# Optimization experiments

Measured on AMD Instinct MI355X. Metric: run time of the kernel, lower is better.

## Reference

```python
import jax, jax.numpy as jnp
import numpy as np
from jax.lax import associative_scan

D_H = 1024

def _binary_operator(e_i, e_j):
    a_i, kv_i = e_i
    a_j, kv_j = e_j
    return (a_j * a_i, a_j * kv_i + kv_j)

def setup_inputs() -> dict:
    key = jax.random.key(0)
    k1, k2 = jax.random.split(key)
    x = jax.random.normal(k1, (4, 4096, 3 * D_H), dtype=jnp.float32)
    carry = jax.random.normal(k2, (4, D_H), dtype=jnp.float32)
    return {"x": x, "carry": carry}

def reference(x, carry):
    d_h = D_H
    inp = jnp.tanh(x[:, :, :d_h])                      # (B, S, d_h)
    gates = jax.nn.sigmoid(x[:, :, d_h:])              # (B, S, 2*d_h)
    input_gate, output_gate = jnp.split(gates, 2, axis=-1)
    forget_gate = 1.0 - input_gate                     # tied gates
    scan_ins = inp * input_gate                        # (B, S, d_h)
    # inject carry at t=0: h_0 = f_0*carry + i_0*in_0
    scan_ins = scan_ins.at[:, 0, :].set(scan_ins[:, 0, :] + carry * forget_gate[:, 0, :])
    _, h = associative_scan(_binary_operator, (forget_gate, scan_ins), axis=1)
    y = jnp.tanh(h) * output_gate                      # (B, S, d_h)
    h_last = h[:, -1, :]
    return (h_last, y)
```

## Files before the change

### kernel.cpp

```cpp
#include <hip/hip_runtime.h>


#define B_SZ 4
#define T_LEN 4096
#define DH 1024
#define ROW4 (3 * DH / 4)
#define CHUNKS 128
#define CLEN (T_LEN / CHUNKS)

__device__ __forceinline__ float fsig(float v) {
    return __builtin_amdgcn_rcpf(1.0f + __expf(-v));
}
__device__ __forceinline__ float ftanh(float v) {
    return 1.0f - 2.0f * __builtin_amdgcn_rcpf(__expf(2.0f * v) + 1.0f);
}

__global__ __launch_bounds__(256) void glru_pass1(const float* __restrict__ x,
                                                  float4* __restrict__ Aag,
                                                  float4* __restrict__ Bag) {
    const int c = blockIdx.x;
    const int b = blockIdx.y;
    const int d4 = threadIdx.x;
    const float4* base = (const float4*)x + (size_t)(b * T_LEN + c * CLEN) * ROW4;

    float4 A = make_float4(1.f, 1.f, 1.f, 1.f);
    float4 Bv = make_float4(0.f, 0.f, 0.f, 0.f);
    for (int t = 0; t < CLEN; ++t) {
        const float4 vi = base[(size_t)t * ROW4 + d4];
        const float4 vg = base[(size_t)t * ROW4 + 256 + d4];
        {
            float ig = fsig(vg.x); float a = 1.f - ig;
            A.x *= a; Bv.x = a * Bv.x + ftanh(vi.x) * ig;
        }
        {
            float ig = fsig(vg.y); float a = 1.f - ig;
            A.y *= a; Bv.y = a * Bv.y + ftanh(vi.y) * ig;
        }
        {
            float ig = fsig(vg.z); float a = 1.f - ig;
            A.z *= a; Bv.z = a * Bv.z + ftanh(vi.z) * ig;
        }
        {
            float ig = fsig(vg.w); float a = 1.f - ig;
            A.w *= a; Bv.w = a * Bv.w + ftanh(vi.w) * ig;
        }
    }
    const int o = (b * CHUNKS + c) * 256 + d4;
    Aag[o] = A;
    Bag[o] = Bv;
}

__global__ __launch_bounds__(256) void glru_pass2(const float* __restrict__ Aag,
                                                  const float* __restrict__ Bag,
                                                  const float* __restrict__ carry,
                                                  float* __restrict__ hinit,
                                                  float* __restrict__ hlast) {
    const int idx = blockIdx.x * 256 + threadIdx.x;
    const int b = idx >> 10;
    const int d = idx & 1023;
    float h = carry[idx];
    #pragma unroll 8
    for (int c = 0; c < CHUNKS; ++c) {
        const int o = (b * CHUNKS + c) * 1024 + d;
        hinit[o] = h;
        h = Aag[o] * h + Bag[o];
    }
    hlast[idx] = h;
}

__global__ __launch_bounds__(256) void glru_pass3(const float* __restrict__ x,
                                                  const float4* __restrict__ hinit,
                                                  float4* __restrict__ y) {
    const int c = blockIdx.x;
    const int b = blockIdx.y;
    const int d4 = threadIdx.x;
    const float4* base = (const float4*)x + (size_t)(b * T_LEN + c * CLEN) * ROW4;
    float4* yb = y + (size_t)(b * T_LEN + c * CLEN) * 256;

    float4 h = hinit[(b * CHUNKS + c) * 256 + d4];
    for (int t = 0; t < CLEN; ++t) {
        const float4 vi = base[(size_t)t * ROW4 + d4];
        const float4 vg = base[(size_t)t * ROW4 + 256 + d4];
        const float4 vo = base[(size_t)t * ROW4 + 512 + d4];
        float4 out;
        {
            float ig = fsig(vg.x); float a = 1.f - ig;
            h.x = a * h.x + ftanh(vi.x) * ig;
            out.x = ftanh(h.x) * fsig(vo.x);
        }
        {
            float ig = fsig(vg.y); float a = 1.f - ig;
            h.y = a * h.y + ftanh(vi.y) * ig;
            out.y = ftanh(h.y) * fsig(vo.y);
        }
        {
            float ig = fsig(vg.z); float a = 1.f - ig;
            h.z = a * h.z + ftanh(vi.z) * ig;
            out.z = ftanh(h.z) * fsig(vo.z);
        }
        {
            float ig = fsig(vg.w); float a = 1.f - ig;
            h.w = a * h.w + ftanh(vi.w) * ig;
            out.w = ftanh(h.w) * fsig(vo.w);
        }
        yb[(size_t)t * 256 + d4] = out;
    }
}

extern "C" void kernel_launch(void* const* d_in, const int* in_sizes, int n_in,
                              void* d_out, int out_size, void* d_ws, size_t ws_size,
                              hipStream_t stream) {
    const float* x = (const float*)d_in[0];
    const float* carry = (const float*)d_in[1];

    float* hlast = (float*)d_out;
    float4* y = (float4*)((float*)d_out + B_SZ * DH);

    float* Aag = (float*)d_ws;
    float* Bag = Aag + (size_t)B_SZ * CHUNKS * DH;
    float* hinit = Bag + (size_t)B_SZ * CHUNKS * DH;

    glru_pass1<<<dim3(CHUNKS, B_SZ), 256, 0, stream>>>(x, (float4*)Aag, (float4*)Bag);
    glru_pass2<<<16, 256, 0, stream>>>(Aag, Bag, carry, hinit, hlast);
    glru_pass3<<<dim3(CHUNKS, B_SZ), 256, 0, stream>>>(x, (const float4*)hinit, y);
}
```

Before: 317.2 us.

## Double the chunk count, software-prefetch next timestep, and use nontemporal y stores

Raises CHUNKS from 128 to 256, which halves the sequential length per block and doubles the grid size for passes 1 and 3 so more waves can hide latency. The inner loops of pass1 and pass3 now load the next timestep's inputs before computing the current one, so load latency overlaps the transcendental math. The y output in pass3 is written with nontemporal stores to keep the streamed output from polluting cache. The cost is a longer serial scan in pass2 (256 chunks), more workspace traffic, and more registers held for the prefetched values.

```diff
diff --git a/kernel.cpp b/kernel.cpp
--- a/kernel.cpp
+++ b/kernel.cpp
@@ -5,8 +5,10 @@
 #define T_LEN 4096
 #define DH 1024
 #define ROW4 (3 * DH / 4)
-#define CHUNKS 128
+#define CHUNKS 256
 #define CLEN (T_LEN / CHUNKS)
+
+typedef float vf4 __attribute__((ext_vector_type(4)));
 
 __device__ __forceinline__ float fsig(float v) {
     return __builtin_amdgcn_rcpf(1.0f + __expf(-v));
@@ -25,9 +27,14 @@
 
     float4 A = make_float4(1.f, 1.f, 1.f, 1.f);
     float4 Bv = make_float4(0.f, 0.f, 0.f, 0.f);
+
+    float4 vi = base[d4];
+    float4 vg = base[256 + d4];
     for (int t = 0; t < CLEN; ++t) {
-        const float4 vi = base[(size_t)t * ROW4 + d4];
-        const float4 vg = base[(size_t)t * ROW4 + 256 + d4];
+        float4 vi_n, vg_n;
+        const int tn = (t + 1 < CLEN) ? (t + 1) : t;
+        vi_n = base[(size_t)tn * ROW4 + d4];
+        vg_n = base[(size_t)tn * ROW4 + 256 + d4];
         {
             float ig = fsig(vg.x); float a = 1.f - ig;
             A.x *= a; Bv.x = a * Bv.x + ftanh(vi.x) * ig;
@@ -44,6 +51,7 @@
             float ig = fsig(vg.w); float a = 1.f - ig;
             A.w *= a; Bv.w = a * Bv.w + ftanh(vi.w) * ig;
         }
+        vi = vi_n; vg = vg_n;
     }
     const int o = (b * CHUNKS + c) * 256 + d4;
     Aag[o] = A;
@@ -70,19 +78,25 @@
 
 __global__ __launch_bounds__(256) void glru_pass3(const float* __restrict__ x,
                                                   const float4* __restrict__ hinit,
-                                                  float4* __restrict__ y) {
+                                                  float* __restrict__ y) {
     const int c = blockIdx.x;
     const int b = blockIdx.y;
     const int d4 = threadIdx.x;
     const float4* base = (const float4*)x + (size_t)(b * T_LEN + c * CLEN) * ROW4;
-    float4* yb = y + (size_t)(b * T_LEN + c * CLEN) * 256;
+    vf4* yb = (vf4*)y + (size_t)(b * T_LEN + c * CLEN) * 256;
 
     float4 h = hinit[(b * CHUNKS + c) * 256 + d4];
+
+    float4 vi = base[d4];
+    float4 vg = base[256 + d4];
+    float4 vo = base[512 + d4];
     for (int t = 0; t < CLEN; ++t) {
-        const float4 vi = base[(size_t)t * ROW4 + d4];
-        const float4 vg = base[(size_t)t * ROW4 + 256 + d4];
-        const float4 vo = base[(size_t)t * ROW4 + 512 + d4];
-        float4 out;
+        float4 vi_n, vg_n, vo_n;
+        const int tn = (t + 1 < CLEN) ? (t + 1) : t;
+        vi_n = base[(size_t)tn * ROW4 + d4];
+        vg_n = base[(size_t)tn * ROW4 + 256 + d4];
+        vo_n = base[(size_t)tn * ROW4 + 512 + d4];
+        vf4 out;
         {
             float ig = fsig(vg.x); float a = 1.f - ig;
             h.x = a * h.x + ftanh(vi.x) * ig;
@@ -103,7 +117,8 @@
             h.w = a * h.w + ftanh(vi.w) * ig;
             out.w = ftanh(h.w) * fsig(vo.w);
         }
-        yb[(size_t)t * 256 + d4] = out;
+        __builtin_nontemporal_store(out, &yb[(size_t)t * 256 + d4]);
+        vi = vi_n; vg = vg_n; vo = vo_n;
     }
 }
 
@@ -114,7 +129,7 @@
     const float* carry = (const float*)d_in[1];
 
     float* hlast = (float*)d_out;
-    float4* y = (float4*)((float*)d_out + B_SZ * DH);
+    float* y = (float*)d_out + B_SZ * DH;
 
     float* Aag = (float*)d_ws;
     float* Bag = Aag + (size_t)B_SZ * CHUNKS * DH;
```

After: 325.3 us. 1.03x slower.

## Fuse three-pass chunked scan into single kernel with decoupled look-back

Applied to the files above, without the earlier changes.

Replaces the three-kernel chunked scan (aggregate, serial carry propagation, recompute) with one fused kernel. Each block publishes its chunk aggregate and, through flags, walks back over earlier chunks to get its starting state. This removes two launches and the serial pass2 kernel. Chunks double to 256, and y is written with nontemporal stores. It relies on blocks being scheduled in roughly increasing order to avoid spin waits or deadlock. x is still read twice per chunk.

```diff
diff --git a/kernel.cpp b/kernel.cpp
--- a/kernel.cpp
+++ b/kernel.cpp
@@ -1,12 +1,18 @@
 #include <hip/hip_runtime.h>
+#include <stdint.h>
 
 
 #define B_SZ 4
 #define T_LEN 4096
 #define DH 1024
 #define ROW4 (3 * DH / 4)
-#define CHUNKS 128
+#define CHUNKS 256
 #define CLEN (T_LEN / CHUNKS)
+
+#define FLAG_AGG 1u
+#define FLAG_INC 2u
+
+typedef float vf4 __attribute__((ext_vector_type(4)));
 
 __device__ __forceinline__ float fsig(float v) {
     return __builtin_amdgcn_rcpf(1.0f + __expf(-v));
@@ -14,96 +20,118 @@
 __device__ __forceinline__ float ftanh(float v) {
     return 1.0f - 2.0f * __builtin_amdgcn_rcpf(__expf(2.0f * v) + 1.0f);
 }
+__device__ __forceinline__ vf4 sig4(vf4 v) {
+    vf4 r; r.x = fsig(v.x); r.y = fsig(v.y); r.z = fsig(v.z); r.w = fsig(v.w); return r;
+}
+__device__ __forceinline__ vf4 tanh4(vf4 v) {
+    vf4 r; r.x = ftanh(v.x); r.y = ftanh(v.y); r.z = ftanh(v.z); r.w = ftanh(v.w); return r;
+}
+struct F2 { float a, b; };
+__device__ __forceinline__ uint64_t pack2(float a, float b) {
+    union { float f[2]; uint64_t u; } u; u.f[0] = a; u.f[1] = b; return u.u;
+}
+__device__ __forceinline__ F2 unpack2(uint64_t v) {
+    union { uint64_t u; float f[2]; } u; u.u = v; return {u.f[0], u.f[1]};
+}
 
-__global__ __launch_bounds__(256) void glru_pass1(const float* __restrict__ x,
-                                                  float4* __restrict__ Aag,
-                                                  float4* __restrict__ Bag) {
-    const int c = blockIdx.x;
-    const int b = blockIdx.y;
+__global__ __launch_bounds__(256) void glru_flags_init(uint32_t* __restrict__ flags) {
+    const int i = blockIdx.x * 256 + threadIdx.x;
+    if (i < B_SZ * CHUNKS) flags[i] = 0u;
+}
+
+__global__ __launch_bounds__(256, 4) void glru_fused(
+    const float* __restrict__ x, const float* __restrict__ carry,
+    uint64_t* __restrict__ AB,
+    uint64_t* __restrict__ Hp,
+    uint32_t* __restrict__ flags,
+    float* __restrict__ hlast,
+    float* __restrict__ y)
+{
+    const int c = blockIdx.x & (CHUNKS - 1);
+    const int b = blockIdx.x >> 8;
     const int d4 = threadIdx.x;
-    const float4* base = (const float4*)x + (size_t)(b * T_LEN + c * CLEN) * ROW4;
+    const vf4* base = (const vf4*)x + (size_t)(b * T_LEN + c * CLEN) * ROW4;
+    const size_t fb = (size_t)b * CHUNKS;
 
-    float4 A = make_float4(1.f, 1.f, 1.f, 1.f);
-    float4 Bv = make_float4(0.f, 0.f, 0.f, 0.f);
+    vf4 A = {1.f, 1.f, 1.f, 1.f};
+    vf4 Bv = {0.f, 0.f, 0.f, 0.f};
+    #pragma unroll 4
     for (int t = 0; t < CLEN; ++t) {
-        const float4 vi = base[(size_t)t * ROW4 + d4];
-        const float4 vg = base[(size_t)t * ROW4 + 256 + d4];
-        {
-            float ig = fsig(vg.x); float a = 1.f - ig;
-            A.x *= a; Bv.x = a * Bv.x + ftanh(vi.x) * ig;
-        }
-        {
-            float ig = fsig(vg.y); float a = 1.f - ig;
-            A.y *= a; Bv.y = a * Bv.y + ftanh(vi.y) * ig;
-        }
-        {
-            float ig = fsig(vg.z); float a = 1.f - ig;
-            A.z *= a; Bv.z = a * Bv.z + ftanh(vi.z) * ig;
-        }
-        {
-            float ig = fsig(vg.w); float a = 1.f - ig;
-            A.w *= a; Bv.w = a * Bv.w + ftanh(vi.w) * ig;
+        vf4 vi = base[(size_t)t * ROW4 + d4];
+        vf4 vg = base[(size_t)t * ROW4 + 256 + d4];
+        vf4 ig = sig4(vg);
+        vf4 a = 1.f - ig;
+        A *= a;
+        Bv = a * Bv + tanh4(vi) * ig;
+    }
+
+    vf4 hin;
+    if (c == 0) {
+        hin = ((const vf4*)carry)[b * 256 + d4];
+    } else {
+        uint64_t* ab = AB + (fb + c) * DH + (size_t)d4 * 4;
+        __hip_atomic_store(&ab[0], pack2(A.x, Bv.x), __ATOMIC_RELAXED, __HIP_MEMORY_SCOPE_AGENT);
+        __hip_atomic_store(&ab[1], pack2(A.y, Bv.y), __ATOMIC_RELAXED, __HIP_MEMORY_SCOPE_AGENT);
+        __hip_atomic_store(&ab[2], pack2(A.z, Bv.z), __ATOMIC_RELAXED, __HIP_MEMORY_SCOPE_AGENT);
+        __hip_atomic_store(&ab[3], pack2(A.w, Bv.w), __ATOMIC_RELAXED, __HIP_MEMORY_SCOPE_AGENT);
+        __syncthreads();
+        if (threadIdx.x == 0)
+            __hip_atomic_store(&flags[fb + c], FLAG_AGG, __ATOMIC_RELEASE, __HIP_MEMORY_SCOPE_AGENT);
+
+        vf4 Ax = {1.f, 1.f, 1.f, 1.f};
+        vf4 Bx = {0.f, 0.f, 0.f, 0.f};
+        int j = c - 1;
+        for (;;) {
+            uint32_t f = __hip_atomic_load(&flags[fb + j], __ATOMIC_ACQUIRE, __HIP_MEMORY_SCOPE_AGENT);
+            if (f == FLAG_INC) {
+                const uint64_t* hp = Hp + (fb + j) * (DH / 2) + (size_t)d4 * 2;
+                uint64_t p0 = __hip_atomic_load(&hp[0], __ATOMIC_RELAXED, __HIP_MEMORY_SCOPE_AGENT);
+                uint64_t p1 = __hip_atomic_load(&hp[1], __ATOMIC_RELAXED, __HIP_MEMORY_SCOPE_AGENT);
+                F2 u0 = unpack2(p0), u1 = unpack2(p1);
+                vf4 hj = {u0.a, u0.b, u1.a, u1.b};
+                hin = Ax * hj + Bx;
+                break;
+            } else if (f == FLAG_AGG) {
+                const uint64_t* abj = AB + (fb + j) * DH + (size_t)d4 * 4;
+                uint64_t q0 = __hip_atomic_load(&abj[0], __ATOMIC_RELAXED, __HIP_MEMORY_SCOPE_AGENT);
+                uint64_t q1 = __hip_atomic_load(&abj[1], __ATOMIC_RELAXED, __HIP_MEMORY_SCOPE_AGENT);
+                uint64_t q2 = __hip_atomic_load(&abj[2], __ATOMIC_RELAXED, __HIP_MEMORY_SCOPE_AGENT);
+                uint64_t q3 = __hip_atomic_load(&abj[3], __ATOMIC_RELAXED, __HIP_MEMORY_SCOPE_AGENT);
+                F2 w0 = unpack2(q0), w1 = unpack2(q1), w2 = unpack2(q2), w3 = unpack2(q3);
+                vf4 Aj = {w0.a, w1.a, w2.a, w3.a};
+                vf4 Bj = {w0.b, w1.b, w2.b, w3.b};
+                Bx = Ax * Bj + Bx;
+                Ax = Ax * Aj;
+                --j;
+            } else {
+                __builtin_amdgcn_s_sleep(2);
+            }
         }
     }
-    const int o = (b * CHUNKS + c) * 256 + d4;
-    Aag[o] = A;
-    Bag[o] = Bv;
-}
 
-__global__ __launch_bounds__(256) void glru_pass2(const float* __restrict__ Aag,
-                                                  const float* __restrict__ Bag,
-                                                  const float* __restrict__ carry,
-                                                  float* __restrict__ hinit,
-                                                  float* __restrict__ hlast) {
-    const int idx = blockIdx.x * 256 + threadIdx.x;
-    const int b = idx >> 10;
-    const int d = idx & 1023;
-    float h = carry[idx];
-    #pragma unroll 8
-    for (int c = 0; c < CHUNKS; ++c) {
-        const int o = (b * CHUNKS + c) * 1024 + d;
-        hinit[o] = h;
-        h = Aag[o] * h + Bag[o];
+    vf4 hend = A * hin + Bv;
+    {
+        uint64_t* hp = Hp + (fb + c) * (DH / 2) + (size_t)d4 * 2;
+        __hip_atomic_store(&hp[0], pack2(hend.x, hend.y), __ATOMIC_RELAXED, __HIP_MEMORY_SCOPE_AGENT);
+        __hip_atomic_store(&hp[1], pack2(hend.z, hend.w), __ATOMIC_RELAXED, __HIP_MEMORY_SCOPE_AGENT);
+        __syncthreads();
+        if (threadIdx.x == 0)
+            __hip_atomic_store(&flags[fb + c], FLAG_INC, __ATOMIC_RELEASE, __HIP_MEMORY_SCOPE_AGENT);
     }
-    hlast[idx] = h;
-}
+    if (c == CHUNKS - 1) ((vf4*)hlast)[b * 256 + d4] = hend;
 
-__global__ __launch_bounds__(256) void glru_pass3(const float* __restrict__ x,
-                                                  const float4* __restrict__ hinit,
-                                                  float4* __restrict__ y) {
-    const int c = blockIdx.x;
-    const int b = blockIdx.y;
-    const int d4 = threadIdx.x;
-    const float4* base = (const float4*)x + (size_t)(b * T_LEN + c * CLEN) * ROW4;
-    float4* yb = y + (size_t)(b * T_LEN + c * CLEN) * 256;
-
-    float4 h = hinit[(b * CHUNKS + c) * 256 + d4];
+    vf4* yb = (vf4*)y + (size_t)(b * T_LEN + c * CLEN) * 256;
+    vf4 h = hin;
+    #pragma unroll 2
     for (int t = 0; t < CLEN; ++t) {
-        const float4 vi = base[(size_t)t * ROW4 + d4];
-        const float4 vg = base[(size_t)t * ROW4 + 256 + d4];
-        const float4 vo = base[(size_t)t * ROW4 + 512 + d4];
-        float4 out;
-        {
-            float ig = fsig(vg.x); float a = 1.f - ig;
-            h.x = a * h.x + ftanh(vi.x) * ig;
-            out.x = ftanh(h.x) * fsig(vo.x);
-        }
-        {
-            float ig = fsig(vg.y); float a = 1.f - ig;
-            h.y = a * h.y + ftanh(vi.y) * ig;
-            out.y = ftanh(h.y) * fsig(vo.y);
-        }
-        {
-            float ig = fsig(vg.z); float a = 1.f - ig;
-            h.z = a * h.z + ftanh(vi.z) * ig;
-            out.z = ftanh(h.z) * fsig(vo.z);
-        }
-        {
-            float ig = fsig(vg.w); float a = 1.f - ig;
-            h.w = a * h.w + ftanh(vi.w) * ig;
-            out.w = ftanh(h.w) * fsig(vo.w);
-        }
-        yb[(size_t)t * 256 + d4] = out;
+        vf4 vi = base[(size_t)t * ROW4 + d4];
+        vf4 vg = base[(size_t)t * ROW4 + 256 + d4];
+        vf4 vo = base[(size_t)t * ROW4 + 512 + d4];
+        vf4 ig = sig4(vg);
+        vf4 a = 1.f - ig;
+        h = a * h + tanh4(vi) * ig;
+        vf4 out = tanh4(h) * sig4(vo);
+        __builtin_nontemporal_store(out, &yb[(size_t)t * 256 + d4]);
     }
 }
 
@@ -114,13 +142,12 @@
     const float* carry = (const float*)d_in[1];
 
     float* hlast = (float*)d_out;
-    float4* y = (float4*)((float*)d_out + B_SZ * DH);
+    float* y = (float*)d_out + B_SZ * DH;
 
-    float* Aag = (float*)d_ws;
-    float* Bag = Aag + (size_t)B_SZ * CHUNKS * DH;
-    float* hinit = Bag + (size_t)B_SZ * CHUNKS * DH;
+    uint64_t* AB = (uint64_t*)d_ws;
+    uint64_t* Hp = AB + (size_t)B_SZ * CHUNKS * DH;
+    uint32_t* flags = (uint32_t*)(Hp + (size_t)B_SZ * CHUNKS * (DH / 2));
 
-    glru_pass1<<<dim3(CHUNKS, B_SZ), 256, 0, stream>>>(x, (float4*)Aag, (float4*)Bag);
-    glru_pass2<<<16, 256, 0, stream>>>(Aag, Bag, carry, hinit, hlast);
-    glru_pass3<<<dim3(CHUNKS, B_SZ), 256, 0, stream>>>(x, (const float4*)hinit, y);
+    glru_flags_init<<<4, 256, 0, stream>>>(flags);
+    glru_fused<<<B_SZ * CHUNKS, 256, 0, stream>>>(x, carry, AB, Hp, flags, hlast, y);
 }
```

After: 944.2 us. +197.7%, slower.
